# Performance work log

Measured on AMD Instinct MI355X. Metric: run time of the kernel, lower is better.

The kernel has to match this reference:

```python
import jax, jax.numpy as jnp
import numpy as np

D = 128; H = 8; L = 6; DFF = 512; EPS = 1e-5; ETA = 1e-3; MAXLEN = 5000


def layernorm(x, g, b):
    m = jnp.mean(x, -1, keepdims=True)
    v = jnp.mean((x - m) ** 2, -1, keepdims=True)
    return (x - m) / jnp.sqrt(v + EPS) * g + b


def mha(q_in, kv_in, Wi, bi, Wo, bo):
    # Wi: [3D, D] packed q/k/v projections (torch in_proj layout)
    dh = D // H
    q = q_in @ Wi[:D].T + bi[:D]
    k = kv_in @ Wi[D:2 * D].T + bi[D:2 * D]
    v = kv_in @ Wi[2 * D:].T + bi[2 * D:]
    B_, Lq, _ = q.shape
    Lk = k.shape[1]
    q = q.reshape(B_, Lq, H, dh)
    k = k.reshape(B_, Lk, H, dh)
    v = v.reshape(B_, Lk, H, dh)
    att = jax.nn.softmax(jnp.einsum('bqhd,bkhd->bhqk', q, k) / jnp.sqrt(jnp.asarray(dh, q.dtype)), axis=-1)
    o = jnp.einsum('bhqk,bkhd->bqhd', att, v).reshape(B_, Lq, D)
    return o @ Wo.T + bo


def posenc(x):
    pos = jnp.arange(MAXLEN, dtype=x.dtype)[:, None]
    div = jnp.exp(jnp.arange(0, D, 2, dtype=x.dtype) * (-jnp.log(jnp.asarray(10000.0, x.dtype)) / D))
    pe = jnp.zeros((MAXLEN, D), x.dtype).at[:, 0::2].set(jnp.sin(pos * div)).at[:, 1::2].set(jnp.cos(pos * div))
    # faithful to original: slices pe by x.size(0) which is the BATCH dim (batch_first tensors)
    return x + pe[: x.shape[0], None, :]


def reference(src, tgt, emb, femb_w, femb_b,
              enc_inw, enc_inb, enc_ow, enc_ob, enc_l1g, enc_l1b, enc_l2g, enc_l2b,
              enc_f1w, enc_f1b, enc_f2w, enc_f2b, enc_ng, enc_nb,
              dec_inw, dec_inb, dec_ow, dec_ob, dec_cinw, dec_cinb, dec_cow, dec_cob,
              dec_l1g, dec_l1b, dec_l2g, dec_l2b, dec_l3g, dec_l3b,
              dec_f1w, dec_f1b, dec_f2w, dec_f2b, dec_ng, dec_nb, fc_w, fc_b):
    scale = jnp.sqrt(jnp.asarray(D, jnp.float32))
    s = posenc(emb[src] * scale)                     # [B,S,D]
    t = posenc((tgt @ femb_w.T + femb_b) * scale)    # [B,T,D]
    mem = s
    for i in range(L):  # encoder (post-norm, ReLU, dropout=0 in eval)
        a = mha(mem, mem, enc_inw[i], enc_inb[i], enc_ow[i], enc_ob[i])
        mem = layernorm(mem + a, enc_l1g[i], enc_l1b[i])
        f = jax.nn.relu(mem @ enc_f1w[i].T + enc_f1b[i]) @ enc_f2w[i].T + enc_f2b[i]
        mem = layernorm(mem + f, enc_l2g[i], enc_l2b[i])
    mem = layernorm(mem, enc_ng, enc_nb)
    y = t
    for i in range(L):  # decoder
        a = mha(y, y, dec_inw[i], dec_inb[i], dec_ow[i], dec_ob[i])
        y = layernorm(y + a, dec_l1g[i], dec_l1b[i])
        c = mha(y, mem, dec_cinw[i], dec_cinb[i], dec_cow[i], dec_cob[i])
        y = layernorm(y + c, dec_l2g[i], dec_l2b[i])
        f = jax.nn.relu(y @ dec_f1w[i].T + dec_f1b[i]) @ dec_f2w[i].T + dec_f2b[i]
        y = layernorm(y + f, dec_l3g[i], dec_l3b[i])
    y = layernorm(y, dec_ng, dec_nb)
    out = y @ fc_w.T + fc_b  # [B,T,1]
    # nn-corrected TN parameter vector: vec + eta * nn_output (pre-final-contract)
    return tgt[..., 0] + ETA * out[..., 0]


def setup_inputs():
    B, S, T = 4, 100, 2048
    ks = iter(jax.random.split(jax.random.key(0), 64))

    def w(shape, s=0.02):
        return jax.random.normal(next(ks), shape, jnp.float32) * s

    inp = {}
    inp['src'] = jax.random.randint(next(ks), (B, S), 0, 2)
    inp['tgt'] = jax.random.normal(next(ks), (B, T, 1), jnp.float32)
    inp['emb'] = w((2, D), 1.0)
    inp['femb_w'] = w((D, 1)); inp['femb_b'] = jnp.zeros((D,))
    inp['enc_inw'] = w((L, 3 * D, D)); inp['enc_inb'] = jnp.zeros((L, 3 * D))
    inp['enc_ow'] = w((L, D, D)); inp['enc_ob'] = jnp.zeros((L, D))
    inp['enc_l1g'] = jnp.ones((L, D)); inp['enc_l1b'] = jnp.zeros((L, D))
    inp['enc_l2g'] = jnp.ones((L, D)); inp['enc_l2b'] = jnp.zeros((L, D))
    inp['enc_f1w'] = w((L, DFF, D)); inp['enc_f1b'] = jnp.zeros((L, DFF))
    inp['enc_f2w'] = w((L, D, DFF)); inp['enc_f2b'] = jnp.zeros((L, D))
    inp['enc_ng'] = jnp.ones((D,)); inp['enc_nb'] = jnp.zeros((D,))
    inp['dec_inw'] = w((L, 3 * D, D)); inp['dec_inb'] = jnp.zeros((L, 3 * D))
    inp['dec_ow'] = w((L, D, D)); inp['dec_ob'] = jnp.zeros((L, D))
    inp['dec_cinw'] = w((L, 3 * D, D)); inp['dec_cinb'] = jnp.zeros((L, 3 * D))
    inp['dec_cow'] = w((L, D, D)); inp['dec_cob'] = jnp.zeros((L, D))
    inp['dec_l1g'] = jnp.ones((L, D)); inp['dec_l1b'] = jnp.zeros((L, D))
    inp['dec_l2g'] = jnp.ones((L, D)); inp['dec_l2b'] = jnp.zeros((L, D))
    inp['dec_l3g'] = jnp.ones((L, D)); inp['dec_l3b'] = jnp.zeros((L, D))
    inp['dec_f1w'] = w((L, DFF, D)); inp['dec_f1b'] = jnp.zeros((L, DFF))
    inp['dec_f2w'] = w((L, D, DFF)); inp['dec_f2b'] = jnp.zeros((L, D))
    inp['dec_ng'] = jnp.ones((D,)); inp['dec_nb'] = jnp.zeros((D,))
    inp['fc_w'] = w((1, D)); inp['fc_b'] = jnp.zeros((1,))
    return inp
```

## Files before the change

kernel.cpp:

```cpp
#include <hip/hip_runtime.h>
#include <hip/hip_bf16.h>
#include <math.h>

#define B_ 4
#define S_ 100
#define T_ 2048
#define DM 128
#define NH 8
#define DH 16
#define NL 6
#define DFFN 512

#define SQRT_D 11.313708498984761f
#define LN10K  9.210340371976184f
#define QSCALE 0.36067376022224085f

typedef _Float16 v4h __attribute__((ext_vector_type(4)));
typedef _Float16 v8h __attribute__((ext_vector_type(8)));
typedef float    v4f __attribute__((ext_vector_type(4)));

__device__ __forceinline__ float fexp2(float x) { return __builtin_amdgcn_exp2f(x); }

__device__ __forceinline__ v4f mfma16(v4h a, v4h b, v4f c) {
    return __builtin_amdgcn_mfma_f32_16x16x16f16(a, b, c, 0, 0, 0);
}

__device__ __forceinline__ void gload_lds16(const void* g, void* l) {
    __builtin_amdgcn_global_load_lds(
        (const __attribute__((address_space(1))) unsigned int*)g,
        (__attribute__((address_space(3))) unsigned int*)l, 16, 0, 0);
}

__device__ __forceinline__ float pe_val(int pos, int d) {
    int i = d >> 1;
    float dv = __expf((float)i * (-2.0f * LN10K / 128.0f));
    float ang = (float)pos * dv;
    return (d & 1) ? __cosf(ang) : __sinf(ang);
}

__global__ __launch_bounds__(256) void conv_w(
    const float* __restrict__ p0, const float* __restrict__ p1,
    const float* __restrict__ p2, const float* __restrict__ p3,
    const float* __restrict__ p4, const float* __restrict__ p5,
    const float* __restrict__ p6, const float* __restrict__ p7,
    const float* __restrict__ p8, const float* __restrict__ p9,
    _Float16* __restrict__ out)
{
    int seg = blockIdx.y;
    const float* s; int sz; long off;
    switch (seg) {
        case 0: s = p0; sz = 294912; off = 0;       break;
        case 1: s = p1; sz = 98304;  off = 294912;  break;
        case 2: s = p2; sz = 393216; off = 393216;  break;
        case 3: s = p3; sz = 393216; off = 786432;  break;
        case 4: s = p4; sz = 294912; off = 1179648; break;
        case 5: s = p5; sz = 98304;  off = 1474560; break;
        case 6: s = p6; sz = 294912; off = 1572864; break;
        case 7: s = p7; sz = 98304;  off = 1867776; break;
        case 8: s = p8; sz = 393216; off = 1966080; break;
        default: s = p9; sz = 393216; off = 2359296; break;
    }
    int idx = (blockIdx.x * 256 + threadIdx.x) * 4;
    if (idx >= sz) return;
    float4 v = *(const float4*)(s + idx);
    v4h h = { (_Float16)v.x, (_Float16)v.y, (_Float16)v.z, (_Float16)v.w };
    *(v4h*)(out + off + idx) = h;
}

__global__ __launch_bounds__(256) void embed_src_kernel(
    const int* __restrict__ src, const float* __restrict__ emb,
    _Float16* __restrict__ outh)
{
    int idx = blockIdx.x * 256 + threadIdx.x;
    if (idx >= B_ * S_ * DM) return;
    int d = idx & 127;
    int row = idx >> 7;
    int b = row / S_;
    int tok = src[row];
    float v = emb[tok * DM + d] * SQRT_D + pe_val(b, d);
    outh[idx] = (_Float16)v;
}

__global__ __launch_bounds__(256) void embed_tgt_kernel(
    const float* __restrict__ tgt, const float* __restrict__ fw,
    const float* __restrict__ fb, _Float16* __restrict__ outh)
{
    int idx = blockIdx.x * 256 + threadIdx.x;
    if (idx >= B_ * T_ * DM) return;
    int d = idx & 127;
    int row = idx >> 7;
    int b = row >> 11;
    float v = (tgt[row] * fw[d] + fb[d]) * SQRT_D + pe_val(b, d);
    outh[idx] = (_Float16)v;
}

template<int MODE>
__global__ __launch_bounds__(256) void gemm_h(
    const _Float16* __restrict__ A, const _Float16* __restrict__ W,
    const float* __restrict__ bias,
    _Float16* __restrict__ Ch,
    _Float16* __restrict__ qo, _Float16* __restrict__ ko, _Float16* __restrict__ vo,
    int M, int N, int K, int L, int Lkp, int part_off, int Lshift,
    long zws, int zbs, long zks, long zvs)
{
    if (MODE == 2) {
        int zi = blockIdx.z;
        W += (size_t)zi * zws;
        bias += (size_t)zi * zbs;
        ko += (size_t)zi * zks;
        vo += (size_t)zi * zvs;
    }
    __shared__ _Float16 As[128][72];
    __shared__ _Float16 Ws[64][72];
    const int t = threadIdx.x;
    const int wave = t >> 6, lane = t & 63;
    const int col16 = lane & 15, grp = lane >> 4;
    const int row0 = blockIdx.x * 128, col0 = blockIdx.y * 64;
    const int wrow0 = (wave >> 1) * 64, wcol0 = (wave & 1) * 32;

    v4f acc[4][2];
    #pragma unroll
    for (int m = 0; m < 4; m++)
        #pragma unroll
        for (int n = 0; n < 2; n++) acc[m][n] = (v4f){0.f, 0.f, 0.f, 0.f};

    for (int k0 = 0; k0 < K; k0 += 64) {
        #pragma unroll
        for (int i = 0; i < 4; i++) {
            int id = i * 256 + t;
            int r = id >> 3, j = id & 7;
            int gr = min(row0 + r, M - 1);
            int4 v = *(const int4*)(A + (size_t)gr * K + k0 + j * 8);
            *(int4*)&As[r][j * 8] = v;
        }
        #pragma unroll
        for (int i = 0; i < 2; i++) {
            int id = i * 256 + t;
            int r = id >> 3, j = id & 7;
            int4 v = *(const int4*)(W + (size_t)(col0 + r) * K + k0 + j * 8);
            *(int4*)&Ws[r][j * 8] = v;
        }
        __syncthreads();
        #pragma unroll
        for (int kk = 0; kk < 4; kk++) {
            v4h a[4], bf[2];
            #pragma unroll
            for (int m = 0; m < 4; m++)
                a[m] = *(const v4h*)&As[wrow0 + m * 16 + col16][kk * 16 + grp * 4];
            #pragma unroll
            for (int n = 0; n < 2; n++)
                bf[n] = *(const v4h*)&Ws[wcol0 + n * 16 + col16][kk * 16 + grp * 4];
            #pragma unroll
            for (int m = 0; m < 4; m++)
                #pragma unroll
                for (int n = 0; n < 2; n++)
                    acc[m][n] = mfma16(a[m], bf[n], acc[m][n]);
        }
        __syncthreads();
    }

    #pragma unroll
    for (int n = 0; n < 2; n++) {
        int gcol = col0 + wcol0 + n * 16 + col16;
        float bv = bias[gcol];
        #pragma unroll
        for (int m = 0; m < 4; m++) {
            int rbase = row0 + wrow0 + m * 16 + grp * 4;
            #pragma unroll
            for (int r = 0; r < 4; r++) {
                int grow = rbase + r;
                if (grow >= M) continue;
                float v = acc[m][n][r] + bv;
                if (MODE == 1) {
                    Ch[(size_t)grow * N + gcol] = (_Float16)fmaxf(v, 0.f);
                } else {
                    int pc = gcol + part_off;
                    int part = pc >> 7;
                    int h = (pc >> 4) & 7;
                    int d = pc & 15;
                    int b = Lshift ? (grow >> Lshift) : (grow / L);
                    int pos = grow - b * L;
                    int bh = b * NH + h;
                    if (part == 0)
                        qo[((size_t)bh * L + pos) * 16 + d] = (_Float16)(v * QSCALE);
                    else if (part == 1)
                        ko[((size_t)bh * L + pos) * 16 + d] = (_Float16)v;
                    else
                        vo[((size_t)bh * 16 + d) * Lkp + pos] = (_Float16)v;
                }
            }
        }
    }
}

template<int MERGE>
__global__ __launch_bounds__(128) void gemm_ln(
    const _Float16* __restrict__ A, const _Float16* __restrict__ W,
    const float* __restrict__ bias, const _Float16* __restrict__ res,
    const float* __restrict__ g, const float* __restrict__ bt,
    const _Float16* __restrict__ po, const float* __restrict__ pm, const float* __restrict__ pl,
    _Float16* __restrict__ youth, int M, int K)
{
    __shared__ _Float16 As[32][72];
    __shared__ _Float16 Ws[128][72];
    const int t = threadIdx.x;
    const int wave = t >> 6, lane = t & 63;
    const int col16 = lane & 15, grp = lane >> 4;
    const int row0 = blockIdx.x * 32;

    v4f acc[8];
    #pragma unroll
    for (int n = 0; n < 8; n++) acc[n] = (v4f){0.f, 0.f, 0.f, 0.f};

    for (int k0 = 0; k0 < K; k0 += 64) {
        #pragma unroll
        for (int i = 0; i < 2; i++) {
            int id = i * 128 + t;
            int r = id >> 3, j = id & 7;
            int grow = min(row0 + r, M - 1);
            if (MERGE) {
                int dim0 = k0 + j * 8;
                int h = dim0 >> 4;
                int doff = dim0 & 8;
                int b = grow >> 11, q = grow & 2047;
                size_t i0 = ((size_t)(b * 2 + 0) * NH + h) * T_ + q;
                size_t i1 = ((size_t)(b * 2 + 1) * NH + h) * T_ + q;
                float m0 = pm[i0], m1 = pm[i1];
                float MM = fmaxf(m0, m1);
                float w0 = fexp2(m0 - MM) * pl[i0];
                float w1 = fexp2(m1 - MM) * pl[i1];
                float inv = 1.0f / (w0 + w1);
                w0 *= inv; w1 *= inv;
                v8h o0 = *(const v8h*)&po[i0 * 16 + doff];
                v8h o1 = *(const v8h*)&po[i1 * 16 + doff];
                v8h mrg;
                #pragma unroll
                for (int e = 0; e < 8; e++)
                    mrg[e] = (_Float16)((float)o0[e] * w0 + (float)o1[e] * w1);
                *(v8h*)&As[r][j * 8] = mrg;
            } else {
                int4 v = *(const int4*)(A + (size_t)grow * K + k0 + j * 8);
                *(int4*)&As[r][j * 8] = v;
            }
        }
        #pragma unroll
        for (int i = 0; i < 8; i++) {
            int id = i * 128 + t;
            int r = id >> 3, j = id & 7;
            int4 v = *(const int4*)(W + (size_t)r * K + k0 + j * 8);
            *(int4*)&Ws[r][j * 8] = v;
        }
        __syncthreads();
        #pragma unroll
        for (int kk = 0; kk < 4; kk++) {
            v4h a = *(const v4h*)&As[wave * 16 + col16][kk * 16 + grp * 4];
            #pragma unroll
            for (int n = 0; n < 8; n++) {
                v4h bf = *(const v4h*)&Ws[n * 16 + col16][kk * 16 + grp * 4];
                acc[n] = mfma16(a, bf, acc[n]);
            }
        }
        __syncthreads();
    }

    float bv[8], gv[8], btv[8];
    #pragma unroll
    for (int n = 0; n < 8; n++) {
        bv[n]  = bias[col16 + 16 * n];
        gv[n]  = g[col16 + 16 * n];
        btv[n] = bt[col16 + 16 * n];
    }
    #pragma unroll
    for (int r = 0; r < 4; r++) {
        int row = row0 + wave * 16 + grp * 4 + r;
        if (row < M) {
            float x[8];
            float sum = 0.f;
            #pragma unroll
            for (int n = 0; n < 8; n++) {
                x[n] = acc[n][r] + bv[n] + (float)res[(size_t)row * DM + col16 + 16 * n];
                sum += x[n];
            }
            sum += __shfl_xor(sum, 1, 64);
            sum += __shfl_xor(sum, 2, 64);
            sum += __shfl_xor(sum, 4, 64);
            sum += __shfl_xor(sum, 8, 64);
            float mean = sum * (1.0f / 128.0f);
            float vs = 0.f;
            #pragma unroll
            for (int n = 0; n < 8; n++) {
                x[n] -= mean;
                vs += x[n] * x[n];
            }
            vs += __shfl_xor(vs, 1, 64);
            vs += __shfl_xor(vs, 2, 64);
            vs += __shfl_xor(vs, 4, 64);
            vs += __shfl_xor(vs, 8, 64);
            float rstd = rsqrtf(vs * (1.0f / 128.0f) + 1e-5f);
            #pragma unroll
            for (int n = 0; n < 8; n++) {
                float o = x[n] * rstd * gv[n] + btv[n];
                youth[(size_t)row * DM + col16 + 16 * n] = (_Float16)o;
            }
        }
    }
}

template<int FINAL>
__global__ __launch_bounds__(256, 6) void attn_p3(
    const _Float16* __restrict__ qh, const _Float16* __restrict__ kh,
    const _Float16* __restrict__ vth, _Float16* __restrict__ outh,
    _Float16* __restrict__ po, float* __restrict__ pm, float* __restrict__ pl,
    int Lq, int Lk, int Lkp, int NS)
{
    __shared__ _Float16 KV[2][2048];
    const int zb = blockIdx.z;
    const int b = zb / NS, split = zb - b * NS;
    const int h = blockIdx.y;
    const int wave = threadIdx.x >> 6, lane = threadIdx.x & 63;
    const int col16 = lane & 15, grp = lane >> 4;
    const int bh = b * NH + h;
    const int qrow = (blockIdx.x * 4 + wave) * 16 + col16;
    const int qcl = min(qrow, Lq - 1);

    v4h q_frag = *(const v4h*)(qh + ((size_t)bh * Lq + qcl) * 16 + grp * 4);
    const char* kbB = (const char*)(kh + (size_t)bh * Lk * 16);
    const char* vbB = (const char*)(vth + (size_t)bh * 16 * Lkp);
    const int LkpB = Lkp * 2;

    const int kvLen = Lk / NS;
    const int kv0 = split * kvLen;
    const int kvEnd = kv0 + kvLen;

    const int krow = wave * 32 + (lane >> 1);
    const long ksrc_off = (long)krow * 32 + (((lane & 1) ^ ((krow >> 2) & 1)) << 4);
    const int vd = (wave & 1) * 8 + (lane >> 3);
    const long vsrc_off = (long)vd * LkpB + (((lane & 7) * 16) ^ ((vd & 7) << 4));
    char* ldsK = (char*)&KV[0][0] + wave * 1024;
    char* ldsV = (char*)&KV[0][0] + 2048 + (wave & 1) * 1024;

    auto stage = [&](int buf, int kc) {
        if (wave < 2)
            gload_lds16(kbB + (long)kc * 32 + ksrc_off, ldsK + buf * 4096);
        else
            gload_lds16(vbB + (long)kc * 2 + vsrc_off, ldsV + buf * 4096);
    };

    const int kxor = (col16 & 4) << 2;

    float m = -1e30f;
    v4f l4 = {0.f, 0.f, 0.f, 0.f};
    v4f oa = {0.f, 0.f, 0.f, 0.f}, ob = {0.f, 0.f, 0.f, 0.f};

    stage(0, kv0);
    __syncthreads();

    int nChunks = (kvLen + 63) >> 6;
    int cur = 0;
    for (int ci = 0; ci < nChunks; ci++, cur ^= 1) {
        int kc = kv0 + ci * 64;
        if (ci + 1 < nChunks) stage(cur ^ 1, kc + 64);

        const char* base = (const char*)&KV[cur][0];
        v4f s4[4];
        #pragma unroll
        for (int sub = 0; sub < 4; sub++) {
            int koff = ((sub * 16 + col16) << 5) + ((grp * 8) ^ kxor);
            v4h k_frag = *(const v4h*)(base + koff);
            s4[sub] = mfma16(k_frag, q_frag, (v4f){0.f, 0.f, 0.f, 0.f});
        }
        if (kc + 64 > kvEnd) {
            #pragma unroll
            for (int sub = 0; sub < 4; sub++)
                #pragma unroll
                for (int r = 0; r < 4; r++) {
                    int key = kc + sub * 16 + grp * 4 + r;
                    if (key >= kvEnd) s4[sub][r] = -1e30f;
                }
        }
        float c0 = fmaxf(fmaxf(s4[0][0], s4[0][1]), fmaxf(s4[0][2], s4[0][3]));
        float c1 = fmaxf(fmaxf(s4[1][0], s4[1][1]), fmaxf(s4[1][2], s4[1][3]));
        float c2 = fmaxf(fmaxf(s4[2][0], s4[2][1]), fmaxf(s4[2][2], s4[2][3]));
        float c3 = fmaxf(fmaxf(s4[3][0], s4[3][1]), fmaxf(s4[3][2], s4[3][3]));
        float cm = fmaxf(fmaxf(c0, c1), fmaxf(c2, c3));
        if (__any(cm > m + 8.0f)) {
            float nm = fmaxf(cm, m);
            nm = fmaxf(nm, __shfl_xor(nm, 16, 64));
            nm = fmaxf(nm, __shfl_xor(nm, 32, 64));
            float corr = fexp2(m - nm);
            l4[0] *= corr; l4[1] *= corr; l4[2] *= corr; l4[3] *= corr;
            oa[0] *= corr; oa[1] *= corr; oa[2] *= corr; oa[3] *= corr;
            ob[0] *= corr; ob[1] *= corr; ob[2] *= corr; ob[3] *= corr;
            m = nm;
        }
        v4h ph[4];
        #pragma unroll
        for (int sub = 0; sub < 4; sub++) {
            float p0 = fexp2(s4[sub][0] - m);
            float p1 = fexp2(s4[sub][1] - m);
            float p2 = fexp2(s4[sub][2] - m);
            float p3 = fexp2(s4[sub][3] - m);
            l4[0] += p0; l4[1] += p1; l4[2] += p2; l4[3] += p3;
            ph[sub] = (v4h){ (_Float16)p0, (_Float16)p1, (_Float16)p2, (_Float16)p3 };
        }
        #pragma unroll
        for (int sub = 0; sub < 4; sub++) {
            int vbyte = 2048 + (col16 << 7) + ((sub * 32 + grp * 8) ^ ((col16 & 7) << 4));
            v4h vt_frag = *(const v4h*)(base + vbyte);
            if (sub & 2)
                ob = mfma16(vt_frag, ph[sub], ob);
            else
                oa = mfma16(vt_frag, ph[sub], oa);
        }
        __syncthreads();
    }

    float l = (l4[0] + l4[1]) + (l4[2] + l4[3]);
    l += __shfl_xor(l, 16, 64);
    l += __shfl_xor(l, 32, 64);
    float inv = 1.0f / l;
    v4f o_acc = {oa[0] + ob[0], oa[1] + ob[1], oa[2] + ob[2], oa[3] + ob[3]};
    if (qrow < Lq) {
        v4h ov = { (_Float16)(o_acc[0] * inv), (_Float16)(o_acc[1] * inv),
                   (_Float16)(o_acc[2] * inv), (_Float16)(o_acc[3] * inv) };
        if (FINAL) {
            *(v4h*)(outh + ((size_t)b * Lq + qrow) * DM + h * DH + grp * 4) = ov;
        } else {
            size_t pidx = ((size_t)zb * NH + h) * Lq + qrow;
            *(v4h*)(po + pidx * 16 + grp * 4) = ov;
            if (grp == 0) { pm[pidx] = m; pl[pidx] = l; }
        }
    }
}

__global__ __launch_bounds__(256) void ln_h(
    _Float16* __restrict__ y, const float* __restrict__ g,
    const float* __restrict__ bta, int M)
{
    int row = blockIdx.x * 4 + (threadIdx.x >> 6);
    int lane = threadIdx.x & 63;
    if (row >= M) return;
    _Float16* yr = y + (size_t)row * DM;
    float x0 = (float)yr[lane], x1 = (float)yr[lane + 64];
    float sum = x0 + x1;
    #pragma unroll
    for (int off = 32; off > 0; off >>= 1) sum += __shfl_xor(sum, off, 64);
    float mean = sum * (1.0f / 128.0f);
    float d0 = x0 - mean, d1 = x1 - mean;
    float vs = d0 * d0 + d1 * d1;
    #pragma unroll
    for (int off = 32; off > 0; off >>= 1) vs += __shfl_xor(vs, off, 64);
    float rstd = rsqrtf(vs * (1.0f / 128.0f) + 1e-5f);
    yr[lane]      = (_Float16)(d0 * rstd * g[lane]      + bta[lane]);
    yr[lane + 64] = (_Float16)(d1 * rstd * g[lane + 64] + bta[lane + 64]);
}

__global__ __launch_bounds__(256) void final_ln_kernel(
    const _Float16* __restrict__ y, const float* __restrict__ tgt,
    const float* __restrict__ g, const float* __restrict__ bta,
    const float* __restrict__ fcw, const float* __restrict__ fcb,
    float* __restrict__ out)
{
    int row = blockIdx.x * 4 + (threadIdx.x >> 6);
    int lane = threadIdx.x & 63;
    const _Float16* yr = y + (size_t)row * DM;
    float x0 = (float)yr[lane], x1 = (float)yr[lane + 64];
    float sum = x0 + x1;
    #pragma unroll
    for (int off = 32; off > 0; off >>= 1) sum += __shfl_xor(sum, off, 64);
    float mean = sum * (1.0f / 128.0f);
    float d0 = x0 - mean, d1 = x1 - mean;
    float vs = d0 * d0 + d1 * d1;
    #pragma unroll
    for (int off = 32; off > 0; off >>= 1) vs += __shfl_xor(vs, off, 64);
    float rstd = rsqrtf(vs * (1.0f / 128.0f) + 1e-5f);
    float o0 = d0 * rstd * g[lane]      + bta[lane];
    float o1 = d1 * rstd * g[lane + 64] + bta[lane + 64];
    float a = o0 * fcw[lane] + o1 * fcw[lane + 64];
    #pragma unroll
    for (int off = 32; off > 0; off >>= 1) a += __shfl_xor(a, off, 64);
    if (lane == 0) out[row] = tgt[row] + 1.0e-3f * (a + fcb[0]);
}

extern "C" void kernel_launch(void* const* d_in, const int* in_sizes, int n_in,
                              void* d_out, int out_size, void* d_ws, size_t ws_size,
                              hipStream_t stream)
{
    (void)in_sizes; (void)n_in; (void)out_size; (void)ws_size;
    const int*   src     = (const int*)  d_in[0];
    const float* tgt     = (const float*)d_in[1];
    const float* emb     = (const float*)d_in[2];
    const float* femb_w  = (const float*)d_in[3];
    const float* femb_b  = (const float*)d_in[4];
    const float* enc_inw = (const float*)d_in[5];
    const float* enc_inb = (const float*)d_in[6];
    const float* enc_ow  = (const float*)d_in[7];
    const float* enc_ob  = (const float*)d_in[8];
    const float* enc_l1g = (const float*)d_in[9];
    const float* enc_l1b = (const float*)d_in[10];
    const float* enc_l2g = (const float*)d_in[11];
    const float* enc_l2b = (const float*)d_in[12];
    const float* enc_f1w = (const float*)d_in[13];
    const float* enc_f1b = (const float*)d_in[14];
    const float* enc_f2w = (const float*)d_in[15];
    const float* enc_f2b = (const float*)d_in[16];
    const float* enc_ng  = (const float*)d_in[17];
    const float* enc_nb  = (const float*)d_in[18];
    const float* dec_inw = (const float*)d_in[19];
    const float* dec_inb = (const float*)d_in[20];
    const float* dec_ow  = (const float*)d_in[21];
    const float* dec_ob  = (const float*)d_in[22];
    const float* dec_cinw= (const float*)d_in[23];
    const float* dec_cinb= (const float*)d_in[24];
    const float* dec_cow = (const float*)d_in[25];
    const float* dec_cob = (const float*)d_in[26];
    const float* dec_l1g = (const float*)d_in[27];
    const float* dec_l1b = (const float*)d_in[28];
    const float* dec_l2g = (const float*)d_in[29];
    const float* dec_l2b = (const float*)d_in[30];
    const float* dec_l3g = (const float*)d_in[31];
    const float* dec_l3b = (const float*)d_in[32];
    const float* dec_f1w = (const float*)d_in[33];
    const float* dec_f1b = (const float*)d_in[34];
    const float* dec_f2w = (const float*)d_in[35];
    const float* dec_f2b = (const float*)d_in[36];
    const float* dec_ng  = (const float*)d_in[37];
    const float* dec_nb  = (const float*)d_in[38];
    const float* fc_w    = (const float*)d_in[39];
    const float* fc_b    = (const float*)d_in[40];

    float* ws = (float*)d_ws;
    float* pm   = ws;
    float* pl   = ws + 131072;
    _Float16* hb = (_Float16*)(ws + 262144);
    _Float16* mem_h  = hb;
    _Float16* ybuf_h = hb + 51200;
    _Float16* aout_h = hb + 1099776;
    _Float16* wh     = hb + 2148352;
    _Float16* po     = hb + 4900864;
    _Float16* BIGH   = hb + 6998016;
    _Float16* QH     = hb + 11192320;
    _Float16* KH     = hb + 12240896;
    _Float16* VTH    = hb + 13289472;
    _Float16* KC     = hb + 14338048;
    _Float16* VC     = hb + 14645248;

    const long W_ENC_INW = 0,       W_ENC_OW = 294912,  W_ENC_F1W = 393216,  W_ENC_F2W = 786432;
    const long W_DEC_INW = 1179648, W_DEC_OW = 1474560, W_DEC_CINW = 1572864, W_DEC_COW = 1867776;
    const long W_DEC_F1W = 1966080, W_DEC_F2W = 2359296;

    conv_w<<<dim3(384, 10), 256, 0, stream>>>(enc_inw, enc_ow, enc_f1w, enc_f2w,
                                              dec_inw, dec_ow, dec_cinw, dec_cow,
                                              dec_f1w, dec_f2w, wh);

    embed_src_kernel<<<200, 256, 0, stream>>>(src, emb, mem_h);
    for (int i = 0; i < NL; i++) {
        gemm_h<2><<<dim3(4, 6), 256, 0, stream>>>(mem_h, wh + W_ENC_INW + i * 49152, enc_inb + i * 384,
            nullptr, QH, KH, VTH, 400, 384, 128, 100, 128, 0, 0, 0, 0, 0, 0);
        attn_p3<1><<<dim3(2, NH, B_), 256, 0, stream>>>(QH, KH, VTH, aout_h,
            nullptr, nullptr, nullptr, 100, 100, 128, 1);
        gemm_ln<0><<<13, 128, 0, stream>>>(aout_h, wh + W_ENC_OW + i * 16384, enc_ob + i * 128,
            mem_h, enc_l1g + i * 128, enc_l1b + i * 128, nullptr, nullptr, nullptr, mem_h, 400, 128);
        gemm_h<1><<<dim3(4, 8), 256, 0, stream>>>(mem_h, wh + W_ENC_F1W + i * 65536, enc_f1b + i * 512,
            BIGH, nullptr, nullptr, nullptr, 400, 512, 128, 0, 0, 0, 0, 0, 0, 0, 0);
        gemm_ln<0><<<13, 128, 0, stream>>>(BIGH, wh + W_ENC_F2W + i * 65536, enc_f2b + i * 128,
            mem_h, enc_l2g + i * 128, enc_l2b + i * 128, nullptr, nullptr, nullptr, mem_h, 400, 512);
    }
    ln_h<<<100, 256, 0, stream>>>(mem_h, enc_ng, enc_nb, 400);
    gemm_h<2><<<dim3(4, 2, 6), 256, 0, stream>>>(mem_h, wh + W_DEC_CINW + 16384, dec_cinb + 128,
        nullptr, nullptr, KC, VC, 400, 256, 128, 100, 128, 128, 0,
        49152, 384, 51200, 65536);

    embed_tgt_kernel<<<4096, 256, 0, stream>>>(tgt, femb_w, femb_b, ybuf_h);
    for (int i = 0; i < NL; i++) {
        gemm_h<2><<<dim3(64, 6), 256, 0, stream>>>(ybuf_h, wh + W_DEC_INW + i * 49152, dec_inb + i * 384,
            nullptr, QH, KH, VTH, 8192, 384, 128, 2048, 2048, 0, 11, 0, 0, 0, 0);
        attn_p3<0><<<dim3(32, NH, B_ * 2), 256, 0, stream>>>(QH, KH, VTH, nullptr,
            po, pm, pl, 2048, 2048, 2048, 2);
        gemm_ln<1><<<256, 128, 0, stream>>>(nullptr, wh + W_DEC_OW + i * 16384, dec_ob + i * 128,
            ybuf_h, dec_l1g + i * 128, dec_l1b + i * 128, po, pm, pl, ybuf_h, 8192, 128);
        gemm_h<2><<<dim3(64, 2), 256, 0, stream>>>(ybuf_h, wh + W_DEC_CINW + i * 49152, dec_cinb + i * 384,
            nullptr, QH, nullptr, nullptr, 8192, 128, 128, 2048, 2048, 0, 11, 0, 0, 0, 0);
        attn_p3<1><<<dim3(32, NH, B_), 256, 0, stream>>>(QH, KC + i * 51200, VC + i * 65536, aout_h,
            nullptr, nullptr, nullptr, 2048, 100, 128, 1);
        gemm_ln<0><<<256, 128, 0, stream>>>(aout_h, wh + W_DEC_COW + i * 16384, dec_cob + i * 128,
            ybuf_h, dec_l2g + i * 128, dec_l2b + i * 128, nullptr, nullptr, nullptr, ybuf_h, 8192, 128);
        gemm_h<1><<<dim3(64, 8), 256, 0, stream>>>(ybuf_h, wh + W_DEC_F1W + i * 65536, dec_f1b + i * 512,
            BIGH, nullptr, nullptr, nullptr, 8192, 512, 128, 0, 0, 0, 0, 0, 0, 0, 0);
        gemm_ln<0><<<256, 128, 0, stream>>>(BIGH, wh + W_DEC_F2W + i * 65536, dec_f2b + i * 128,
            ybuf_h, dec_l3g + i * 128, dec_l3b + i * 128, nullptr, nullptr, nullptr, ybuf_h, 8192, 512);
    }
    final_ln_kernel<<<2048, 256, 0, stream>>>(ybuf_h, tgt, dec_ng, dec_nb, fc_w, fc_b, (float*)d_out);
}
```

Before: 856.5 us.

## Fuse FFN into one kernel and cross-attention block into one kernel

Adds ffn_ln, which computes FF1+ReLU+FF2+residual+LayerNorm per 32-row tile and keeps the hidden activations in shared memory, so the 8192x512 intermediate is never written to global memory. Adds cross_ln, which fuses the Q projection, cross-attention over the 100 cached keys, the output projection and the residual LayerNorm into one kernel per 32-row tile. Both cut decoder launches and global round trips. In exchange each block re-streams all weights and only 256 blocks of 128 threads run, which may leave the GPU underoccupied and serialise the weight loads.

```diff
diff --git a/kernel.cpp b/kernel.cpp
--- a/kernel.cpp
+++ b/kernel.cpp
@@ -302,6 +302,325 @@
                 float o = x[n] * rstd * gv[n] + btv[n];
                 youth[(size_t)row * DM + col16 + 16 * n] = (_Float16)o;
             }
+        }
+    }
+}
+
+__global__ __launch_bounds__(128) void ffn_ln(
+    const _Float16* __restrict__ A, const _Float16* __restrict__ W1,
+    const float* __restrict__ b1, const _Float16* __restrict__ W2,
+    const float* __restrict__ b2, const _Float16* __restrict__ res,
+    const float* __restrict__ g, const float* __restrict__ bt,
+    _Float16* __restrict__ youth, int M)
+{
+    __shared__ _Float16 As[32][136];
+    __shared__ _Float16 W1s[64][136];
+    __shared__ _Float16 Hs[32][72];
+    __shared__ _Float16 W2s[128][72];
+    const int t = threadIdx.x;
+    const int wave = t >> 6, lane = t & 63;
+    const int col16 = lane & 15, grp = lane >> 4;
+    const int row0 = blockIdx.x * 32;
+
+    #pragma unroll
+    for (int rd = 0; rd < 4; rd++) {
+        int id = rd * 128 + t;
+        int r = id >> 4, j = id & 15;
+        int grow = min(row0 + r, M - 1);
+        int4 v = *(const int4*)(A + (size_t)grow * DM + j * 8);
+        *(int4*)&As[r][j * 8] = v;
+    }
+
+    v4f oacc[8];
+    #pragma unroll
+    for (int n = 0; n < 8; n++) oacc[n] = (v4f){0.f, 0.f, 0.f, 0.f};
+    __syncthreads();
+
+    for (int hc = 0; hc < 8; hc++) {
+        #pragma unroll
+        for (int rd = 0; rd < 8; rd++) {
+            int id = rd * 128 + t;
+            int r = id >> 4, j = id & 15;
+            int4 v = *(const int4*)(W1 + (size_t)(hc * 64 + r) * DM + j * 8);
+            *(int4*)&W1s[r][j * 8] = v;
+        }
+        #pragma unroll
+        for (int rd = 0; rd < 8; rd++) {
+            int id = rd * 128 + t;
+            int r = id >> 3, j = id & 7;
+            int4 v = *(const int4*)(W2 + (size_t)r * DFFN + hc * 64 + j * 8);
+            *(int4*)&W2s[r][j * 8] = v;
+        }
+        __syncthreads();
+        v4f hacc[4];
+        #pragma unroll
+        for (int n = 0; n < 4; n++) hacc[n] = (v4f){0.f, 0.f, 0.f, 0.f};
+        #pragma unroll
+        for (int kk = 0; kk < 8; kk++) {
+            v4h a = *(const v4h*)&As[wave * 16 + col16][kk * 16 + grp * 4];
+            #pragma unroll
+            for (int n = 0; n < 4; n++) {
+                v4h bf = *(const v4h*)&W1s[n * 16 + col16][kk * 16 + grp * 4];
+                hacc[n] = mfma16(a, bf, hacc[n]);
+            }
+        }
+        #pragma unroll
+        for (int n = 0; n < 4; n++) {
+            float bb = b1[hc * 64 + n * 16 + col16];
+            #pragma unroll
+            for (int r = 0; r < 4; r++) {
+                float h = fmaxf(hacc[n][r] + bb, 0.f);
+                Hs[wave * 16 + grp * 4 + r][n * 16 + col16] = (_Float16)h;
+            }
+        }
+        #pragma unroll
+        for (int kk = 0; kk < 4; kk++) {
+            v4h a = *(const v4h*)&Hs[wave * 16 + col16][kk * 16 + grp * 4];
+            #pragma unroll
+            for (int n = 0; n < 8; n++) {
+                v4h bf = *(const v4h*)&W2s[n * 16 + col16][kk * 16 + grp * 4];
+                oacc[n] = mfma16(a, bf, oacc[n]);
+            }
+        }
+        __syncthreads();
+    }
+
+    float bv[8], gv[8], btv[8];
+    #pragma unroll
+    for (int n = 0; n < 8; n++) {
+        bv[n]  = b2[col16 + 16 * n];
+        gv[n]  = g[col16 + 16 * n];
+        btv[n] = bt[col16 + 16 * n];
+    }
+    #pragma unroll
+    for (int r = 0; r < 4; r++) {
+        int row = row0 + wave * 16 + grp * 4 + r;
+        if (row < M) {
+            float x[8];
+            float sum = 0.f;
+            #pragma unroll
+            for (int n = 0; n < 8; n++) {
+                x[n] = oacc[n][r] + bv[n] + (float)res[(size_t)row * DM + col16 + 16 * n];
+                sum += x[n];
+            }
+            sum += __shfl_xor(sum, 1, 64);
+            sum += __shfl_xor(sum, 2, 64);
+            sum += __shfl_xor(sum, 4, 64);
+            sum += __shfl_xor(sum, 8, 64);
+            float mean = sum * (1.0f / 128.0f);
+            float vs = 0.f;
+            #pragma unroll
+            for (int n = 0; n < 8; n++) {
+                x[n] -= mean;
+                vs += x[n] * x[n];
+            }
+            vs += __shfl_xor(vs, 1, 64);
+            vs += __shfl_xor(vs, 2, 64);
+            vs += __shfl_xor(vs, 4, 64);
+            vs += __shfl_xor(vs, 8, 64);
+            float rstd = rsqrtf(vs * (1.0f / 128.0f) + 1e-5f);
+            #pragma unroll
+            for (int n = 0; n < 8; n++) {
+                float o = x[n] * rstd * gv[n] + btv[n];
+                youth[(size_t)row * DM + col16 + 16 * n] = (_Float16)o;
+            }
+        }
+    }
+}
+
+__global__ __launch_bounds__(128) void cross_ln(
+    const _Float16* __restrict__ y, const _Float16* __restrict__ Wq,
+    const float* __restrict__ bq, const _Float16* __restrict__ KC_l,
+    const _Float16* __restrict__ VC_l, const _Float16* __restrict__ Wo,
+    const float* __restrict__ bo, const float* __restrict__ g,
+    const float* __restrict__ bt, _Float16* __restrict__ youth)
+{
+    __shared__ _Float16 YO[32][136];
+    __shared__ _Float16 Qs[32][136];
+    __shared__ _Float16 Ws[128][72];
+    __shared__ _Float16 Khs[128 * 16];
+    __shared__ _Float16 Vhs[16 * 128];
+    const int t = threadIdx.x;
+    const int wave = t >> 6, lane = t & 63;
+    const int col16 = lane & 15, grp = lane >> 4;
+    const int row0 = blockIdx.x * 32;
+    const int b = row0 >> 11;
+
+    #pragma unroll
+    for (int rd = 0; rd < 4; rd++) {
+        int id = rd * 128 + t;
+        int r = id >> 4, j = id & 15;
+        int4 v = *(const int4*)(y + (size_t)(row0 + r) * DM + j * 8);
+        *(int4*)&YO[r][j * 8] = v;
+    }
+    __syncthreads();
+
+    {
+        v4f qacc[8];
+        #pragma unroll
+        for (int n = 0; n < 8; n++) qacc[n] = (v4f){0.f, 0.f, 0.f, 0.f};
+        for (int k0 = 0; k0 < 128; k0 += 64) {
+            #pragma unroll
+            for (int i = 0; i < 8; i++) {
+                int id = i * 128 + t;
+                int r = id >> 3, j = id & 7;
+                int4 v = *(const int4*)(Wq + (size_t)r * DM + k0 + j * 8);
+                *(int4*)&Ws[r][j * 8] = v;
+            }
+            __syncthreads();
+            #pragma unroll
+            for (int kk = 0; kk < 4; kk++) {
+                v4h a = *(const v4h*)&YO[wave * 16 + col16][k0 + kk * 16 + grp * 4];
+                #pragma unroll
+                for (int n = 0; n < 8; n++) {
+                    v4h bf = *(const v4h*)&Ws[n * 16 + col16][kk * 16 + grp * 4];
+                    qacc[n] = mfma16(a, bf, qacc[n]);
+                }
+            }
+            __syncthreads();
+        }
+        #pragma unroll
+        for (int n = 0; n < 8; n++) {
+            float bb = bq[n * 16 + col16];
+            #pragma unroll
+            for (int r = 0; r < 4; r++)
+                Qs[wave * 16 + grp * 4 + r][n * 16 + col16] =
+                    (_Float16)((qacc[n][r] + bb) * QSCALE);
+        }
+    }
+
+    const char* kbB = (const char*)(KC_l + (size_t)(b * NH) * S_ * DH);
+    const char* vbB = (const char*)(VC_l + (size_t)(b * NH) * DH * 128);
+    for (int h = 0; h < NH; h++) {
+        __syncthreads();
+        #pragma unroll
+        for (int rd = 0; rd < 2; rd++) {
+            int dst = rd * 2048 + t * 16;
+            int krow = (dst >> 5);
+            int half = (t & 1);
+            gload_lds16(kbB + (long)h * 3200 + (long)krow * 32 +
+                        ((half ^ ((krow >> 2) & 1)) << 4),
+                        (char*)Khs + rd * 2048);
+        }
+        #pragma unroll
+        for (int rd = 0; rd < 2; rd++) {
+            int dst = rd * 2048 + t * 16;
+            int vd = dst >> 8;
+            int inoff = (t & 15) * 16;
+            gload_lds16(vbB + (long)h * 4096 + (long)vd * 256 +
+                        (inoff ^ ((vd & 7) << 4)),
+                        (char*)Vhs + rd * 2048);
+        }
+        __syncthreads();
+
+        v4h q_frag = *(const v4h*)&Qs[wave * 16 + col16][h * 16 + grp * 4];
+        const int kxor = (col16 & 4) << 2;
+        v4f s4[7];
+        #pragma unroll
+        for (int sub = 0; sub < 7; sub++) {
+            int koff = ((sub * 16 + col16) << 5) + ((grp * 8) ^ kxor);
+            v4h k_frag = *(const v4h*)((const char*)Khs + koff);
+            s4[sub] = mfma16(k_frag, q_frag, (v4f){0.f, 0.f, 0.f, 0.f});
+        }
+        #pragma unroll
+        for (int r = 0; r < 4; r++) {
+            int key = 96 + grp * 4 + r;
+            if (key >= S_) s4[6][r] = -1e30f;
+        }
+        float mx = -1e30f;
+        #pragma unroll
+        for (int sub = 0; sub < 7; sub++)
+            #pragma unroll
+            for (int r = 0; r < 4; r++) mx = fmaxf(mx, s4[sub][r]);
+        mx = fmaxf(mx, __shfl_xor(mx, 16, 64));
+        mx = fmaxf(mx, __shfl_xor(mx, 32, 64));
+        float l = 0.f;
+        float p[7][4];
+        #pragma unroll
+        for (int sub = 0; sub < 7; sub++)
+            #pragma unroll
+            for (int r = 0; r < 4; r++) {
+                p[sub][r] = fexp2(s4[sub][r] - mx);
+                l += p[sub][r];
+            }
+        l += __shfl_xor(l, 16, 64);
+        l += __shfl_xor(l, 32, 64);
+        float inv = 1.0f / l;
+        v4f o = {0.f, 0.f, 0.f, 0.f};
+        #pragma unroll
+        for (int sub = 0; sub < 7; sub++) {
+            v4h ph = { (_Float16)(p[sub][0] * inv), (_Float16)(p[sub][1] * inv),
+                       (_Float16)(p[sub][2] * inv), (_Float16)(p[sub][3] * inv) };
+            int vbyte = (col16 << 8) + ((sub * 32 + grp * 8) ^ ((col16 & 7) << 4));
+            v4h vt = *(const v4h*)((const char*)Vhs + vbyte);
+            o = mfma16(vt, ph, o);
+        }
+        #pragma unroll
+        for (int r = 0; r < 4; r++)
+            YO[wave * 16 + col16][h * 16 + grp * 4 + r] = (_Float16)o[r];
+    }
+    __syncthreads();
+
+    v4f acc[8];
+    #pragma unroll
+    for (int n = 0; n < 8; n++) acc[n] = (v4f){0.f, 0.f, 0.f, 0.f};
+    for (int k0 = 0; k0 < 128; k0 += 64) {
+        #pragma unroll
+        for (int i = 0; i < 8; i++) {
+            int id = i * 128 + t;
+            int r = id >> 3, j = id & 7;
+            int4 v = *(const int4*)(Wo + (size_t)r * DM + k0 + j * 8);
+            *(int4*)&Ws[r][j * 8] = v;
+        }
+        __syncthreads();
+        #pragma unroll
+        for (int kk = 0; kk < 4; kk++) {
+            v4h a = *(const v4h*)&YO[wave * 16 + col16][k0 + kk * 16 + grp * 4];
+            #pragma unroll
+            for (int n = 0; n < 8; n++) {
+                v4h bf = *(const v4h*)&Ws[n * 16 + col16][kk * 16 + grp * 4];
+                acc[n] = mfma16(a, bf, acc[n]);
+            }
+        }
+        __syncthreads();
+    }
+    float bv[8], gv[8], btv[8];
+    #pragma unroll
+    for (int n = 0; n < 8; n++) {
+        bv[n]  = bo[col16 + 16 * n];
+        gv[n]  = g[col16 + 16 * n];
+        btv[n] = bt[col16 + 16 * n];
+    }
+    #pragma unroll
+    for (int r = 0; r < 4; r++) {
+        int row = row0 + wave * 16 + grp * 4 + r;
+        float x[8];
+        float sum = 0.f;
+        #pragma unroll
+        for (int n = 0; n < 8; n++) {
+            x[n] = acc[n][r] + bv[n] + (float)youth[(size_t)row * DM + col16 + 16 * n];
+            sum += x[n];
+        }
+        sum += __shfl_xor(sum, 1, 64);
+        sum += __shfl_xor(sum, 2, 64);
+        sum += __shfl_xor(sum, 4, 64);
+        sum += __shfl_xor(sum, 8, 64);
+        float mean = sum * (1.0f / 128.0f);
+        float vs = 0.f;
+        #pragma unroll
+        for (int n = 0; n < 8; n++) {
+            x[n] -= mean;
+            vs += x[n] * x[n];
+        }
+        vs += __shfl_xor(vs, 1, 64);
+        vs += __shfl_xor(vs, 2, 64);
+        vs += __shfl_xor(vs, 4, 64);
+        vs += __shfl_xor(vs, 8, 64);
+        float rstd = rsqrtf(vs * (1.0f / 128.0f) + 1e-5f);
+        #pragma unroll
+        for (int n = 0; n < 8; n++) {
+            float oo = x[n] * rstd * gv[n] + btv[n];
+            youth[(size_t)row * DM + col16 + 16 * n] = (_Float16)oo;
         }
     }
 }
@@ -538,7 +857,6 @@
     _Float16* aout_h = hb + 1099776;
     _Float16* wh     = hb + 2148352;
     _Float16* po     = hb + 4900864;
-    _Float16* BIGH   = hb + 6998016;
     _Float16* QH     = hb + 11192320;
     _Float16* KH     = hb + 12240896;
     _Float16* VTH    = hb + 13289472;
@@ -561,10 +879,9 @@
             nullptr, nullptr, nullptr, 100, 100, 128, 1);
         gemm_ln<0><<<13, 128, 0, stream>>>(aout_h, wh + W_ENC_OW + i * 16384, enc_ob + i * 128,
             mem_h, enc_l1g + i * 128, enc_l1b + i * 128, nullptr, nullptr, nullptr, mem_h, 400, 128);
-        gemm_h<1><<<dim3(4, 8), 256, 0, stream>>>(mem_h, wh + W_ENC_F1W + i * 65536, enc_f1b + i * 512,
-            BIGH, nullptr, nullptr, nullptr, 400, 512, 128, 0, 0, 0, 0, 0, 0, 0, 0);
-        gemm_ln<0><<<13, 128, 0, stream>>>(BIGH, wh + W_ENC_F2W + i * 65536, enc_f2b + i * 128,
-            mem_h, enc_l2g + i * 128, enc_l2b + i * 128, nullptr, nullptr, nullptr, mem_h, 400, 512);
+        ffn_ln<<<13, 128, 0, stream>>>(mem_h, wh + W_ENC_F1W + i * 65536, enc_f1b + i * 512,
+            wh + W_ENC_F2W + i * 65536, enc_f2b + i * 128,
+            mem_h, enc_l2g + i * 128, enc_l2b + i * 128, mem_h, 400);
     }
     ln_h<<<100, 256, 0, stream>>>(mem_h, enc_ng, enc_nb, 400);
     gemm_h<2><<<dim3(4, 2, 6), 256, 0, stream>>>(mem_h, wh + W_DEC_CINW + 16384, dec_cinb + 128,
@@ -579,16 +896,12 @@
             po, pm, pl, 2048, 2048, 2048, 2);
         gemm_ln<1><<<256, 128, 0, stream>>>(nullptr, wh + W_DEC_OW + i * 16384, dec_ob + i * 128,
             ybuf_h, dec_l1g + i * 128, dec_l1b + i * 128, po, pm, pl, ybuf_h, 8192, 128);
-        gemm_h<2><<<dim3(64, 2), 256, 0, stream>>>(ybuf_h, wh + W_DEC_CINW + i * 49152, dec_cinb + i * 384,
-            nullptr, QH, nullptr, nullptr, 8192, 128, 128, 2048, 2048, 0, 11, 0, 0, 0, 0);
-        attn_p3<1><<<dim3(32, NH, B_), 256, 0, stream>>>(QH, KC + i * 51200, VC + i * 65536, aout_h,
-            nullptr, nullptr, nullptr, 2048, 100, 128, 1);
-        gemm_ln<0><<<256, 128, 0, stream>>>(aout_h, wh + W_DEC_COW + i * 16384, dec_cob + i * 128,
-            ybuf_h, dec_l2g + i * 128, dec_l2b + i * 128, nullptr, nullptr, nullptr, ybuf_h, 8192, 128);
-        gemm_h<1><<<dim3(64, 8), 256, 0, stream>>>(ybuf_h, wh + W_DEC_F1W + i * 65536, dec_f1b + i * 512,
-            BIGH, nullptr, nullptr, nullptr, 8192, 512, 128, 0, 0, 0, 0, 0, 0, 0, 0);
-        gemm_ln<0><<<256, 128, 0, stream>>>(BIGH, wh + W_DEC_F2W + i * 65536, dec_f2b + i * 128,
-            ybuf_h, dec_l3g + i * 128, dec_l3b + i * 128, nullptr, nullptr, nullptr, ybuf_h, 8192, 512);
+        cross_ln<<<256, 128, 0, stream>>>(ybuf_h, wh + W_DEC_CINW + i * 49152, dec_cinb + i * 384,
+            KC + i * 51200, VC + i * 65536, wh + W_DEC_COW + i * 16384, dec_cob + i * 128,
+            dec_l2g + i * 128, dec_l2b + i * 128, ybuf_h);
+        ffn_ln<<<256, 128, 0, stream>>>(ybuf_h, wh + W_DEC_F1W + i * 65536, dec_f1b + i * 512,
+            wh + W_DEC_F2W + i * 65536, dec_f2b + i * 128,
+            ybuf_h, dec_l3g + i * 128, dec_l3b + i * 128, ybuf_h, 8192);
     }
     final_ln_kernel<<<2048, 256, 0, stream>>>(ybuf_h, tgt, dec_ng, dec_nb, fc_w, fc_b, (float*)d_out);
 }
```

Measured after the change: 797.1 us. -6.9%, faster.
